# Performance work log

Measured on AMD Instinct MI355X. Metric: run time of the kernel, lower is better.

Reference implementation:

```python
import jax, jax.numpy as jnp
import numpy as np

STATE_DIM = 1024
INPUT_DIM = 1024
OUTPUT_DIM = 1024
BATCH = 8
SEQ = 2048


def setup_inputs() -> dict:
    key = jax.random.key(0)
    k_x, k_a, k_b, k_w, k_bias = jax.random.split(key, 5)
    x = jax.random.normal(k_x, (BATCH, SEQ, INPUT_DIM), dtype=jnp.float32)
    # diagonal transition a in (0, 0.99) for stability
    A = jax.random.uniform(k_a, (STATE_DIM,), dtype=jnp.float32, minval=0.0, maxval=0.99)
    B = jax.random.normal(k_b, (STATE_DIM, INPUT_DIM), dtype=jnp.float32) / np.sqrt(INPUT_DIM)
    W = jax.random.normal(k_w, (OUTPUT_DIM, STATE_DIM), dtype=jnp.float32) / np.sqrt(STATE_DIM)
    b = jax.random.normal(k_bias, (OUTPUT_DIM,), dtype=jnp.float32) * 0.01
    return {"x": x, "A": A, "B": B, "W": W, "b": b}


def reference(x, A, B, W, b):
    # x: [batch, seq, input_dim]
    # Input projection: u_t = B x_t  -> [batch, seq, state_dim]
    u = jnp.einsum('bld,nd->bln', x, B)
    # Diagonal linear recurrence h_t = A * h_{t-1} + u_t via associative scan.
    # Pair representation (a, b) composes as (a1*a2, a2*b1 + b2).
    aa = jnp.broadcast_to(A, u.shape)

    def combine(c1, c2):
        a1, b1 = c1
        a2, b2 = c2
        return a1 * a2, a2 * b1 + b2

    _, h = jax.lax.associative_scan(combine, (aa, u), axis=1)
    # Output projection: [batch, seq, output_dim]
    return jnp.einsum('bln,on->blo', h, W) + b
```

## Files before the change

kernel.cpp:

```cpp
#include <hip/hip_runtime.h>
#include <stdint.h>

#define BATCH 8
#define SEQ 2048
#define DIM 1024
#define MTOT (BATCH * SEQ)
#define NCHUNK 64
#define CLEN (SEQ / NCHUNK)

typedef __attribute__((ext_vector_type(8))) short short8;
typedef __attribute__((ext_vector_type(8))) unsigned short ushort8;
typedef __attribute__((ext_vector_type(4))) float floatx4;


__device__ __forceinline__ unsigned short f2bf(float f) {
  union { float f; unsigned u; } c; c.f = f;
  unsigned u = c.u;
  return (unsigned short)((u + 0x7FFFu + ((u >> 16) & 1u)) >> 16);
}
__device__ __forceinline__ float bf2f(unsigned short h) {
  union { unsigned u; float f; } c; c.u = ((unsigned)h) << 16;
  return c.f;
}

__device__ __forceinline__ void gll16(const void* g, void* l) {
  __builtin_amdgcn_global_load_lds(
      (__attribute__((address_space(1))) void*)(uintptr_t)g,
      (__attribute__((address_space(3))) void*)(uintptr_t)l,
      16, 0, 0);
}


#define XN8 (MTOT * DIM / 8)
#define MN8 (DIM * DIM / 8)

__global__ __launch_bounds__(256) void cast3_kernel(
    const float* __restrict__ x, const float* __restrict__ B,
    const float* __restrict__ W, unsigned short* __restrict__ xb,
    unsigned short* __restrict__ Bb, unsigned short* __restrict__ Wb) {
  int i = blockIdx.x * 256 + threadIdx.x;
  const float* src;
  unsigned short* dst;
  int li;
  if (i < XN8) {
    src = x; dst = xb; li = i;
  } else if (i < XN8 + MN8) {
    src = B; dst = Bb; li = i - XN8;
  } else {
    src = W; dst = Wb; li = i - XN8 - MN8;
  }
  const float4* s4 = (const float4*)src;
  float4 a = s4[2 * li], b = s4[2 * li + 1];
  uint4 o;
  o.x = (unsigned)f2bf(a.x) | ((unsigned)f2bf(a.y) << 16);
  o.y = (unsigned)f2bf(a.z) | ((unsigned)f2bf(a.w) << 16);
  o.z = (unsigned)f2bf(b.x) | ((unsigned)f2bf(b.y) << 16);
  o.w = (unsigned)f2bf(b.z) | ((unsigned)f2bf(b.w) << 16);
  ((uint4*)dst)[li] = o;
}


template <bool OUT_BF16>
__global__ __launch_bounds__(256) void gemm_nt(
    const unsigned short* __restrict__ A,
    const unsigned short* __restrict__ B,
    void* __restrict__ Cp,
    const float* __restrict__ bias,
    int K, int N) {
  __shared__ unsigned short smem[16384];
  unsigned short* sA = smem;
  unsigned short* sB = smem + 8192;

  const int tid = threadIdx.x;
  const int wave = tid >> 6, lane = tid & 63;

  const int id = blockIdx.x;
  const int xcd = id & 7, j = id >> 3;
  const int mt = xcd * 16 + (j >> 3);
  const int nt = j & 7;
  const size_t m0 = (size_t)mt * 128;
  const int n0 = nt * 128;

  floatx4 acc[4][4] = {};

  const int srow = wave * 8 + (lane >> 3);
  const int scol = (((lane & 7) ^ ((lane >> 3) & 7)) * 8);
  const unsigned short* gA = A + (m0 + srow) * (size_t)K + scol;
  const unsigned short* gB = B + ((size_t)n0 + srow) * (size_t)K + scol;
  unsigned short* lA = sA + wave * 8 * 64;
  unsigned short* lB = sB + wave * 8 * 64;

  const int fr = lane & 15;
  const int frs = fr & 7;
  const int kb = lane >> 4;
  const int wm = (wave & 1) * 64, wn = (wave >> 1) * 64;

  for (int kt = 0; kt < K; kt += 64) {
#pragma unroll
    for (int r = 0; r < 4; ++r) {
      gll16(gA + (size_t)r * 32 * K + kt, lA + r * 32 * 64);
      gll16(gB + (size_t)r * 32 * K + kt, lB + r * 32 * 64);
    }
    asm volatile("s_waitcnt vmcnt(0)" ::: "memory");
    __syncthreads();
#pragma unroll
    for (int kk = 0; kk < 64; kk += 32) {
      short8 af[4], bfv[4];
#pragma unroll
      for (int i = 0; i < 4; ++i)
        af[i] = *(const short8*)(sA + (wm + i * 16 + fr) * 64 +
                                 ((((kk >> 3) + kb) ^ frs) * 8));
#pragma unroll
      for (int jj = 0; jj < 4; ++jj)
        bfv[jj] = *(const short8*)(sB + (wn + jj * 16 + fr) * 64 +
                                   ((((kk >> 3) + kb) ^ frs) * 8));
#pragma unroll
      for (int i = 0; i < 4; ++i)
#pragma unroll
        for (int jj = 0; jj < 4; ++jj)
          acc[i][jj] = __builtin_amdgcn_mfma_f32_16x16x32_bf16(
              af[i], bfv[jj], acc[i][jj], 0, 0, 0);
    }
    __syncthreads();
  }

  const int col = lane & 15;
  const int row4 = (lane >> 4) * 4;

  if (OUT_BF16) {
    unsigned short* sC = smem;
#pragma unroll
    for (int i = 0; i < 4; ++i)
#pragma unroll
      for (int jj = 0; jj < 4; ++jj)
#pragma unroll
        for (int r = 0; r < 4; ++r)
          sC[(wm + i * 16 + row4 + r) * 128 + wn + jj * 16 + col] =
              f2bf(acc[i][jj][r]);
    __syncthreads();
    unsigned short* C = (unsigned short*)Cp;
#pragma unroll
    for (int s = 0; s < 8; ++s) {
      int row = wave * 32 + s * 4 + (lane >> 4);
      int c8 = (lane & 15) * 8;
      *(ushort8*)(C + (m0 + row) * (size_t)N + n0 + c8) =
          *(const ushort8*)(sC + row * 128 + c8);
    }
  } else {
    float* C = (float*)Cp;
#pragma unroll
    for (int i = 0; i < 4; ++i) {
#pragma unroll
      for (int jj = 0; jj < 4; ++jj) {
#pragma unroll
        for (int r = 0; r < 4; ++r) {
          size_t m = m0 + wm + i * 16 + row4 + r;
          int n = n0 + wn + jj * 16 + col;
          C[m * N + n] = acc[i][jj][r] + bias[n];
        }
      }
    }
  }
}


__global__ __launch_bounds__(256) void scan_carry(
    const unsigned short* __restrict__ u, const float* __restrict__ A,
    float* __restrict__ carry) {
  const int n0 = threadIdx.x * 8;
  const int c = blockIdx.x * 2 + threadIdx.y;
  const int b = blockIdx.y;
  float a[8], s[8];
  *(float4*)&a[0] = *(const float4*)(A + n0);
  *(float4*)&a[4] = *(const float4*)(A + n0 + 4);
#pragma unroll
  for (int i = 0; i < 8; ++i) s[i] = 0.f;
  size_t base = ((size_t)(b * SEQ + c * CLEN)) * DIM + n0;
#pragma unroll 4
  for (int t = 0; t < CLEN; ++t) {
    ushort8 v = *(const ushort8*)(u + base + (size_t)t * DIM);
#pragma unroll
    for (int i = 0; i < 8; ++i) s[i] = fmaf(a[i], s[i], bf2f(v[i]));
  }
  float* dst = carry + ((size_t)b * NCHUNK + c) * DIM + n0;
  *(float4*)dst = *(float4*)&s[0];
  *(float4*)(dst + 4) = *(float4*)&s[4];
}

__global__ __launch_bounds__(256) void scan_combine(
    float* __restrict__ carry, const float* __restrict__ A) {
  const int id = blockIdx.x * 256 + threadIdx.x;
  const int b = id >> 10, n = id & (DIM - 1);
  float a = A[n];
  float aL = a;
#pragma unroll
  for (int i = 0; i < 5; ++i) aL *= aL;
  float s = 0.f;
  for (int c = 0; c < NCHUNK; ++c) {
    size_t idx = ((size_t)b * NCHUNK + c) * DIM + n;
    float local = carry[idx];
    carry[idx] = s;
    s = fmaf(aL, s, local);
  }
}

__global__ __launch_bounds__(256) void scan_apply(
    unsigned short* __restrict__ u, const float* __restrict__ A,
    const float* __restrict__ carry) {
  const int n0 = threadIdx.x * 8;
  const int c = blockIdx.x * 2 + threadIdx.y;
  const int b = blockIdx.y;
  float a[8], s[8];
  *(float4*)&a[0] = *(const float4*)(A + n0);
  *(float4*)&a[4] = *(const float4*)(A + n0 + 4);
  const float* cin = carry + ((size_t)b * NCHUNK + c) * DIM + n0;
  *(float4*)&s[0] = *(const float4*)cin;
  *(float4*)&s[4] = *(const float4*)(cin + 4);
  size_t base = ((size_t)(b * SEQ + c * CLEN)) * DIM + n0;
#pragma unroll 4
  for (int t = 0; t < CLEN; ++t) {
    size_t idx = base + (size_t)t * DIM;
    ushort8 v = *(const ushort8*)(u + idx);
    ushort8 o;
#pragma unroll
    for (int i = 0; i < 8; ++i) {
      s[i] = fmaf(a[i], s[i], bf2f(v[i]));
      o[i] = f2bf(s[i]);
    }
    *(ushort8*)(u + idx) = o;
  }
}


extern "C" void kernel_launch(void* const* d_in, const int* in_sizes, int n_in,
                              void* d_out, int out_size, void* d_ws,
                              size_t ws_size, hipStream_t stream) {
  const float* x    = (const float*)d_in[0];
  const float* A    = (const float*)d_in[1];
  const float* B    = (const float*)d_in[2];
  const float* W    = (const float*)d_in[3];
  const float* bias = (const float*)d_in[4];

  char* ws = (char*)d_ws;
  unsigned short* xb = (unsigned short*)ws;
  float* carry       = (float*)ws;
  unsigned short* u  = (unsigned short*)(ws + 33554432);
  unsigned short* Bb = (unsigned short*)(ws + 67108864);
  unsigned short* Wb = (unsigned short*)(ws + 69206016);

  cast3_kernel<<<(XN8 + 2 * MN8) / 256, 256, 0, stream>>>(x, B, W, xb, Bb, Wb);

  gemm_nt<true><<<(MTOT / 128) * (DIM / 128), 256, 0, stream>>>(
      xb, Bb, (void*)u, nullptr, DIM, DIM);

  scan_carry<<<dim3(NCHUNK / 2, BATCH), dim3(128, 2), 0, stream>>>(u, A, carry);
  scan_combine<<<(BATCH * DIM) / 256, 256, 0, stream>>>(carry, A);
  scan_apply<<<dim3(NCHUNK / 2, BATCH), dim3(128, 2), 0, stream>>>(u, A, carry);

  gemm_nt<false><<<(MTOT / 128) * (DIM / 128), 256, 0, stream>>>(
      u, Wb, d_out, bias, DIM, DIM);
}
```

Measured before the change: 236.9 us.

## Fuse input GEMM with chunked scan using decoupled lookback and in-kernel x cast

```diff
diff --git a/kernel.cpp b/kernel.cpp
--- a/kernel.cpp
+++ b/kernel.cpp
@@ -5,8 +5,8 @@
 #define SEQ 2048
 #define DIM 1024
 #define MTOT (BATCH * SEQ)
-#define NCHUNK 64
-#define CLEN (SEQ / NCHUNK)
+#define NM 16
+#define NTILE 8
 
 typedef __attribute__((ext_vector_type(8))) short short8;
 typedef __attribute__((ext_vector_type(8))) unsigned short ushort8;
@@ -30,25 +30,25 @@
       16, 0, 0);
 }
 
-
-#define XN8 (MTOT * DIM / 8)
+__device__ __forceinline__ unsigned pkbf(float f1, float f0) {
+  return __builtin_amdgcn_perm(__builtin_bit_cast(unsigned, f1),
+                               __builtin_bit_cast(unsigned, f0), 0x07060302u);
+}
+
+
 #define MN8 (DIM * DIM / 8)
 
-__global__ __launch_bounds__(256) void cast3_kernel(
-    const float* __restrict__ x, const float* __restrict__ B,
-    const float* __restrict__ W, unsigned short* __restrict__ xb,
-    unsigned short* __restrict__ Bb, unsigned short* __restrict__ Wb) {
+__global__ __launch_bounds__(256) void castBW_kernel(
+    const float* __restrict__ B, const float* __restrict__ W,
+    unsigned short* __restrict__ Bb, unsigned short* __restrict__ Wb,
+    unsigned* __restrict__ flags ) {
   int i = blockIdx.x * 256 + threadIdx.x;
-  const float* src;
-  unsigned short* dst;
-  int li;
-  if (i < XN8) {
-    src = x; dst = xb; li = i;
-  } else if (i < XN8 + MN8) {
-    src = B; dst = Bb; li = i - XN8;
-  } else {
-    src = W; dst = Wb; li = i - XN8 - MN8;
-  }
+  if (blockIdx.x == 0) {
+    for (int w = threadIdx.x; w < 1025; w += 256) flags[w] = 0u;
+  }
+  const float* src; unsigned short* dst; int li;
+  if (i < MN8) { src = B; dst = Bb; li = i; }
+  else         { src = W; dst = Wb; li = i - MN8; }
   const float4* s4 = (const float4*)src;
   float4 a = s4[2 * li], b = s4[2 * li + 1];
   uint4 o;
@@ -60,13 +60,194 @@
 }
 
 
-template <bool OUT_BF16>
-__global__ __launch_bounds__(256) void gemm_nt(
+__global__ __launch_bounds__(256) void gemm1_scan(
+    const float* __restrict__ x, const unsigned short* __restrict__ Bb,
+    const float* __restrict__ Adiag, unsigned short* __restrict__ h,
+    float* __restrict__ aggbuf, unsigned* __restrict__ flags,
+    unsigned* __restrict__ ticket) {
+  __shared__ __align__(16) char smem[49152];
+  float* sAf = (float*)smem;
+  unsigned short* sBu = (unsigned short*)(smem + 32768);
+  __shared__ unsigned tkt;
+
+  const int tid = threadIdx.x;
+  const int wave = tid >> 6, lane = tid & 63;
+
+  if (tid == 0) tkt = atomicAdd(ticket, 1u);
+  __syncthreads();
+  const unsigned id = tkt;
+  const int c = id >> 6;
+  const int b = id & 7;
+  const int nt = (id >> 3) & 7;
+  const int mt = b * NM + c;
+  const size_t m0 = (size_t)mt * 128;
+  const int n0 = nt * 128;
+
+  floatx4 acc[4][4] = {};
+
+  unsigned offA[8];
+#pragma unroll
+  for (int r = 0; r < 8; ++r) {
+    int row = wave * 32 + r * 4 + (lane >> 4);
+    int blk = (lane & 15) ^ (row & 15);
+    offA[r] = (unsigned)(row * 4096 + blk * 16);
+  }
+  unsigned offB[4];
+#pragma unroll
+  for (int r = 0; r < 4; ++r) {
+    int row = r * 32 + wave * 8 + (lane >> 3);
+    int blk = (lane & 7) ^ ((lane >> 3) & 7);
+    offB[r] = (unsigned)(row * 2048 + blk * 16);
+  }
+  const char* baseA = (const char*)(x + m0 * 1024);
+  const char* baseB = (const char*)(Bb + (size_t)n0 * 1024);
+
+  const int fr = lane & 15;
+  const int kb = lane >> 4;
+  const int wm = (wave & 1) * 64, wn = (wave >> 1) * 64;
+
+  for (int kt = 0; kt < 1024; kt += 64) {
+#pragma unroll
+    for (int r = 0; r < 8; ++r)
+      gll16(baseA + offA[r], smem + (wave * 32 + r * 4) * 256);
+#pragma unroll
+    for (int r = 0; r < 4; ++r)
+      gll16(baseB + offB[r], (char*)sBu + (wave * 8 + r * 32) * 128);
+    baseA += 256;
+    baseB += 128;
+    asm volatile("s_waitcnt vmcnt(0)" ::: "memory");
+    __syncthreads();
+#pragma unroll
+    for (int kk = 0; kk < 64; kk += 32) {
+      short8 af[4], bfv[4];
+#pragma unroll
+      for (int i = 0; i < 4; ++i) {
+        const float* pA = sAf + (wm + i * 16 + fr) * 64;
+        int bb0 = (kk >> 2) + kb * 2;
+        float4 lo = *(const float4*)(pA + ((bb0 ^ fr) << 2));
+        float4 hi = *(const float4*)(pA + (((bb0 + 1) ^ fr) << 2));
+        union { short8 s; uint4 u; } cv;
+        cv.u.x = pkbf(lo.y, lo.x);
+        cv.u.y = pkbf(lo.w, lo.z);
+        cv.u.z = pkbf(hi.y, hi.x);
+        cv.u.w = pkbf(hi.w, hi.z);
+        af[i] = cv.s;
+      }
+#pragma unroll
+      for (int jj = 0; jj < 4; ++jj)
+        bfv[jj] = *(const short8*)(sBu + (wn + jj * 16 + fr) * 64 +
+                                   ((((kk >> 3) + kb) ^ (fr & 7)) * 8));
+#pragma unroll
+      for (int i = 0; i < 4; ++i)
+#pragma unroll
+        for (int jj = 0; jj < 4; ++jj)
+          acc[i][jj] = __builtin_amdgcn_mfma_f32_16x16x32_bf16(
+              af[i], bfv[jj], acc[i][jj], 0, 0, 0);
+    }
+    __syncthreads();
+  }
+
+  unsigned short* sC = (unsigned short*)smem;
+  float* segsum = (float*)(smem + 32768);
+  float* aLs    = (float*)(smem + 32768 + 1024);
+  float* l2as   = (float*)(smem + 32768 + 1536);
+  float* carryB = (float*)(smem + 32768 + 2048);
+
+  const int col = lane & 15;
+  const int row4 = (lane >> 4) * 4;
+#pragma unroll
+  for (int i = 0; i < 4; ++i)
+#pragma unroll
+    for (int jj = 0; jj < 4; ++jj)
+#pragma unroll
+      for (int r = 0; r < 4; ++r)
+        sC[(wm + i * 16 + row4 + r) * 128 + wn + jj * 16 + col] =
+            f2bf(acc[i][jj][r]);
+  __syncthreads();
+
+  {
+    const int n = tid & 127, seg = tid >> 7;
+    const float a = Adiag[n0 + n];
+    float s = 0.f;
+    int t0 = seg * 64;
+#pragma unroll 8
+    for (int t = 0; t < 64; ++t) {
+      s = fmaf(a, s, bf2f(sC[(t0 + t) * 128 + n]));
+      sC[(t0 + t) * 128 + n] = f2bf(s);
+    }
+    segsum[seg * 128 + n] = s;
+    if (seg == 0) {
+      float a2 = a * a, a4 = a2 * a2, a8 = a4 * a4, a16 = a8 * a8;
+      float a32 = a16 * a16;
+      aLs[n] = a32 * a32;
+      l2as[n] = __builtin_amdgcn_logf(a);
+    }
+  }
+  __syncthreads();
+
+  if (tid < 128) {
+    aggbuf[(size_t)mt * 1024 + n0 + tid] =
+        segsum[128 + tid] + aLs[tid] * segsum[tid];
+  }
+  __syncthreads();
+  if (tid == 0)
+    __hip_atomic_store(&flags[mt * 8 + nt], 1u, __ATOMIC_RELEASE,
+                       __HIP_MEMORY_SCOPE_AGENT);
+
+  if (tid < 128) {
+    float aL128 = aLs[tid] * aLs[tid];
+    float cb = 0.f;
+    for (int p = 0; p < c; ++p) {
+      const int fi = (b * NM + p) * 8 + nt;
+      while (__hip_atomic_load(&flags[fi], __ATOMIC_ACQUIRE,
+                               __HIP_MEMORY_SCOPE_AGENT) == 0u)
+        __builtin_amdgcn_s_sleep(2);
+      cb = fmaf(aL128, cb, aggbuf[(size_t)(b * NM + p) * 1024 + n0 + tid]);
+    }
+    carryB[tid] = cb;
+  }
+  __syncthreads();
+
+  {
+    const int nb = (lane & 15) * 8;
+    const int seg = wave >> 1;
+    float cf[8], l2[8], a4v[8], apow[8];
+#pragma unroll
+    for (int j = 0; j < 8; ++j) {
+      int n = nb + j;
+      float cb = carryB[n];
+      cf[j] = seg ? fmaf(aLs[n], cb, segsum[n]) : cb;
+      l2[j] = l2as[n];
+      float a = Adiag[n0 + n];
+      float a2 = a * a;
+      a4v[j] = a2 * a2;
+    }
+    const int rr0 = (wave & 1) * 32 + (lane >> 4);
+#pragma unroll
+    for (int j = 0; j < 8; ++j)
+      apow[j] = __builtin_amdgcn_exp2f(l2[j] * (float)(rr0 + 1));
+    unsigned short* hout = h + (m0 + wave * 32) * 1024 + n0 + nb;
+#pragma unroll
+    for (int s = 0; s < 8; ++s) {
+      int row = wave * 32 + s * 4 + (lane >> 4);
+      ushort8 loc = *(const ushort8*)(sC + row * 128 + nb);
+      ushort8 o;
+#pragma unroll
+      for (int j = 0; j < 8; ++j) {
+        float v = fmaf(apow[j], cf[j], bf2f(loc[j]));
+        o[j] = f2bf(v);
+        apow[j] *= a4v[j];
+      }
+      *(ushort8*)(hout + (size_t)(s * 4 + (lane >> 4)) * 1024) = o;
+    }
+  }
+}
+
+
+__global__ __launch_bounds__(256) void gemm2(
     const unsigned short* __restrict__ A,
     const unsigned short* __restrict__ B,
-    void* __restrict__ Cp,
-    const float* __restrict__ bias,
-    int K, int N) {
+    float* __restrict__ C, const float* __restrict__ bias) {
   __shared__ unsigned short smem[16384];
   unsigned short* sA = smem;
   unsigned short* sB = smem + 8192;
@@ -85,8 +266,8 @@
 
   const int srow = wave * 8 + (lane >> 3);
   const int scol = (((lane & 7) ^ ((lane >> 3) & 7)) * 8);
-  const unsigned short* gA = A + (m0 + srow) * (size_t)K + scol;
-  const unsigned short* gB = B + ((size_t)n0 + srow) * (size_t)K + scol;
+  const unsigned short* gA = A + (m0 + srow) * 1024 + scol;
+  const unsigned short* gB = B + ((size_t)n0 + srow) * 1024 + scol;
   unsigned short* lA = sA + wave * 8 * 64;
   unsigned short* lB = sB + wave * 8 * 64;
 
@@ -95,11 +276,11 @@
   const int kb = lane >> 4;
   const int wm = (wave & 1) * 64, wn = (wave >> 1) * 64;
 
-  for (int kt = 0; kt < K; kt += 64) {
+  for (int kt = 0; kt < 1024; kt += 64) {
 #pragma unroll
     for (int r = 0; r < 4; ++r) {
-      gll16(gA + (size_t)r * 32 * K + kt, lA + r * 32 * 64);
-      gll16(gB + (size_t)r * 32 * K + kt, lB + r * 32 * 64);
+      gll16(gA + (size_t)r * 32 * 1024 + kt, lA + r * 32 * 64);
+      gll16(gB + (size_t)r * 32 * 1024 + kt, lB + r * 32 * 64);
     }
     asm volatile("s_waitcnt vmcnt(0)" ::: "memory");
     __syncthreads();
@@ -126,109 +307,16 @@
 
   const int col = lane & 15;
   const int row4 = (lane >> 4) * 4;
-
-  if (OUT_BF16) {
-    unsigned short* sC = smem;
-#pragma unroll
-    for (int i = 0; i < 4; ++i)
-#pragma unroll
-      for (int jj = 0; jj < 4; ++jj)
-#pragma unroll
-        for (int r = 0; r < 4; ++r)
-          sC[(wm + i * 16 + row4 + r) * 128 + wn + jj * 16 + col] =
-              f2bf(acc[i][jj][r]);
-    __syncthreads();
-    unsigned short* C = (unsigned short*)Cp;
-#pragma unroll
-    for (int s = 0; s < 8; ++s) {
-      int row = wave * 32 + s * 4 + (lane >> 4);
-      int c8 = (lane & 15) * 8;
-      *(ushort8*)(C + (m0 + row) * (size_t)N + n0 + c8) =
-          *(const ushort8*)(sC + row * 128 + c8);
-    }
-  } else {
-    float* C = (float*)Cp;
-#pragma unroll
-    for (int i = 0; i < 4; ++i) {
-#pragma unroll
-      for (int jj = 0; jj < 4; ++jj) {
-#pragma unroll
-        for (int r = 0; r < 4; ++r) {
-          size_t m = m0 + wm + i * 16 + row4 + r;
-          int n = n0 + wn + jj * 16 + col;
-          C[m * N + n] = acc[i][jj][r] + bias[n];
-        }
+#pragma unroll
+  for (int i = 0; i < 4; ++i)
+#pragma unroll
+    for (int jj = 0; jj < 4; ++jj)
+#pragma unroll
+      for (int r = 0; r < 4; ++r) {
+        size_t m = m0 + wm + i * 16 + row4 + r;
+        int n = n0 + wn + jj * 16 + col;
+        C[m * 1024 + n] = acc[i][jj][r] + bias[n];
       }
-    }
-  }
-}
-
-
-__global__ __launch_bounds__(256) void scan_carry(
-    const unsigned short* __restrict__ u, const float* __restrict__ A,
-    float* __restrict__ carry) {
-  const int n0 = threadIdx.x * 8;
-  const int c = blockIdx.x * 2 + threadIdx.y;
-  const int b = blockIdx.y;
-  float a[8], s[8];
-  *(float4*)&a[0] = *(const float4*)(A + n0);
-  *(float4*)&a[4] = *(const float4*)(A + n0 + 4);
-#pragma unroll
-  for (int i = 0; i < 8; ++i) s[i] = 0.f;
-  size_t base = ((size_t)(b * SEQ + c * CLEN)) * DIM + n0;
-#pragma unroll 4
-  for (int t = 0; t < CLEN; ++t) {
-    ushort8 v = *(const ushort8*)(u + base + (size_t)t * DIM);
-#pragma unroll
-    for (int i = 0; i < 8; ++i) s[i] = fmaf(a[i], s[i], bf2f(v[i]));
-  }
-  float* dst = carry + ((size_t)b * NCHUNK + c) * DIM + n0;
-  *(float4*)dst = *(float4*)&s[0];
-  *(float4*)(dst + 4) = *(float4*)&s[4];
-}
-
-__global__ __launch_bounds__(256) void scan_combine(
-    float* __restrict__ carry, const float* __restrict__ A) {
-  const int id = blockIdx.x * 256 + threadIdx.x;
-  const int b = id >> 10, n = id & (DIM - 1);
-  float a = A[n];
-  float aL = a;
-#pragma unroll
-  for (int i = 0; i < 5; ++i) aL *= aL;
-  float s = 0.f;
-  for (int c = 0; c < NCHUNK; ++c) {
-    size_t idx = ((size_t)b * NCHUNK + c) * DIM + n;
-    float local = carry[idx];
-    carry[idx] = s;
-    s = fmaf(aL, s, local);
-  }
-}
-
-__global__ __launch_bounds__(256) void scan_apply(
-    unsigned short* __restrict__ u, const float* __restrict__ A,
-    const float* __restrict__ carry) {
-  const int n0 = threadIdx.x * 8;
-  const int c = blockIdx.x * 2 + threadIdx.y;
-  const int b = blockIdx.y;
-  float a[8], s[8];
-  *(float4*)&a[0] = *(const float4*)(A + n0);
-  *(float4*)&a[4] = *(const float4*)(A + n0 + 4);
-  const float* cin = carry + ((size_t)b * NCHUNK + c) * DIM + n0;
-  *(float4*)&s[0] = *(const float4*)cin;
-  *(float4*)&s[4] = *(const float4*)(cin + 4);
-  size_t base = ((size_t)(b * SEQ + c * CLEN)) * DIM + n0;
-#pragma unroll 4
-  for (int t = 0; t < CLEN; ++t) {
-    size_t idx = base + (size_t)t * DIM;
-    ushort8 v = *(const ushort8*)(u + idx);
-    ushort8 o;
-#pragma unroll
-    for (int i = 0; i < 8; ++i) {
-      s[i] = fmaf(a[i], s[i], bf2f(v[i]));
-      o[i] = f2bf(s[i]);
-    }
-    *(ushort8*)(u + idx) = o;
-  }
 }
 
 
@@ -242,21 +330,17 @@
   const float* bias = (const float*)d_in[4];
 
   char* ws = (char*)d_ws;
-  unsigned short* xb = (unsigned short*)ws;
-  float* carry       = (float*)ws;
-  unsigned short* u  = (unsigned short*)(ws + 33554432);
-  unsigned short* Bb = (unsigned short*)(ws + 67108864);
-  unsigned short* Wb = (unsigned short*)(ws + 69206016);
-
-  cast3_kernel<<<(XN8 + 2 * MN8) / 256, 256, 0, stream>>>(x, B, W, xb, Bb, Wb);
-
-  gemm_nt<true><<<(MTOT / 128) * (DIM / 128), 256, 0, stream>>>(
-      xb, Bb, (void*)u, nullptr, DIM, DIM);
-
-  scan_carry<<<dim3(NCHUNK / 2, BATCH), dim3(128, 2), 0, stream>>>(u, A, carry);
-  scan_combine<<<(BATCH * DIM) / 256, 256, 0, stream>>>(carry, A);
-  scan_apply<<<dim3(NCHUNK / 2, BATCH), dim3(128, 2), 0, stream>>>(u, A, carry);
-
-  gemm_nt<false><<<(MTOT / 128) * (DIM / 128), 256, 0, stream>>>(
-      u, Wb, d_out, bias, DIM, DIM);
-}
+  unsigned short* hbuf = (unsigned short*)ws;
+  unsigned short* Bb = (unsigned short*)(ws + 33554432);
+  unsigned short* Wb = (unsigned short*)(ws + 35651584);
+  float* aggbuf = (float*)(ws + 37748736);
+  unsigned* flags = (unsigned*)(ws + 38273024);
+  unsigned* ticket = flags + 1024;
+
+  castBW_kernel<<<2 * MN8 / 256, 256, 0, stream>>>(B, W, Bb, Wb, flags);
+
+  gemm1_scan<<<128 * NTILE, 256, 0, stream>>>(x, Bb, A, hbuf, aggbuf, flags,
+                                              ticket);
+
+  gemm2<<<128 * NTILE, 256, 0, stream>>>(hbuf, Wb, (float*)d_out, bias);
+}
```

Measured after the change: 458.6 us. 93.6% more time.

## Replace three-pass chunked scan with single-pass decoupled-lookback scan kernel

Applied to the files above, without the earlier changes.

```diff
diff --git a/kernel.cpp b/kernel.cpp
--- a/kernel.cpp
+++ b/kernel.cpp
@@ -5,8 +5,8 @@
 #define SEQ 2048
 #define DIM 1024
 #define MTOT (BATCH * SEQ)
-#define NCHUNK 64
-#define CLEN (SEQ / NCHUNK)
+#define SC_CH 64
+#define SC_T 32
 
 typedef __attribute__((ext_vector_type(8))) short short8;
 typedef __attribute__((ext_vector_type(8))) unsigned short ushort8;
@@ -37,8 +37,12 @@
 __global__ __launch_bounds__(256) void cast3_kernel(
     const float* __restrict__ x, const float* __restrict__ B,
     const float* __restrict__ W, unsigned short* __restrict__ xb,
-    unsigned short* __restrict__ Bb, unsigned short* __restrict__ Wb) {
+    unsigned short* __restrict__ Bb, unsigned short* __restrict__ Wb,
+    unsigned* __restrict__ flags ) {
   int i = blockIdx.x * 256 + threadIdx.x;
+  if (blockIdx.x == 0) {
+    for (int w = threadIdx.x; w < 544; w += 256) flags[w] = 0u;
+  }
   const float* src;
   unsigned short* dst;
   int li;
@@ -164,70 +168,111 @@
 }
 
 
-__global__ __launch_bounds__(256) void scan_carry(
-    const unsigned short* __restrict__ u, const float* __restrict__ A,
-    float* __restrict__ carry) {
-  const int n0 = threadIdx.x * 8;
-  const int c = blockIdx.x * 2 + threadIdx.y;
-  const int b = blockIdx.y;
-  float a[8], s[8];
-  *(float4*)&a[0] = *(const float4*)(A + n0);
-  *(float4*)&a[4] = *(const float4*)(A + n0 + 4);
-#pragma unroll
-  for (int i = 0; i < 8; ++i) s[i] = 0.f;
-  size_t base = ((size_t)(b * SEQ + c * CLEN)) * DIM + n0;
-#pragma unroll 4
-  for (int t = 0; t < CLEN; ++t) {
+__global__ __launch_bounds__(256, 2) void scan_lb(
+    unsigned short* __restrict__ u, const float* __restrict__ Adiag,
+    float* __restrict__ aggbuf, unsigned* __restrict__ flags,
+    unsigned* __restrict__ ticket) {
+  __shared__ float sHalf0[1024];
+  __shared__ float sCarry[1024];
+  __shared__ unsigned svid;
+
+  const int tid = threadIdx.x;
+  if (tid == 0) svid = atomicAdd(ticket, 1u);
+  __syncthreads();
+  const unsigned vid = svid;
+  const int b = vid & 7;
+  const int c = vid >> 3;
+  const int half = tid >> 7;
+  const int ch0 = (tid & 127) * 8;
+  const int lane = tid & 63;
+
+  float a[8], a16[8], aL[8];
+  *(float4*)&a[0] = *(const float4*)(Adiag + ch0);
+  *(float4*)&a[4] = *(const float4*)(Adiag + ch0 + 4);
+#pragma unroll
+  for (int j = 0; j < 8; ++j) {
+    float t = a[j];
+    t *= t; t *= t; t *= t; t *= t;
+    a16[j] = t;
+    aL[j] = t * t;
+  }
+
+  const size_t base = ((size_t)(b * SEQ + c * SC_T + half * 16)) * DIM + ch0;
+  ushort8 rv[16];
+  float s[8];
+#pragma unroll
+  for (int j = 0; j < 8; ++j) s[j] = 0.f;
+#pragma unroll
+  for (int t = 0; t < 16; ++t) {
     ushort8 v = *(const ushort8*)(u + base + (size_t)t * DIM);
 #pragma unroll
-    for (int i = 0; i < 8; ++i) s[i] = fmaf(a[i], s[i], bf2f(v[i]));
-  }
-  float* dst = carry + ((size_t)b * NCHUNK + c) * DIM + n0;
-  *(float4*)dst = *(float4*)&s[0];
-  *(float4*)(dst + 4) = *(float4*)&s[4];
-}
-
-__global__ __launch_bounds__(256) void scan_combine(
-    float* __restrict__ carry, const float* __restrict__ A) {
-  const int id = blockIdx.x * 256 + threadIdx.x;
-  const int b = id >> 10, n = id & (DIM - 1);
-  float a = A[n];
-  float aL = a;
-#pragma unroll
-  for (int i = 0; i < 5; ++i) aL *= aL;
-  float s = 0.f;
-  for (int c = 0; c < NCHUNK; ++c) {
-    size_t idx = ((size_t)b * NCHUNK + c) * DIM + n;
-    float local = carry[idx];
-    carry[idx] = s;
-    s = fmaf(aL, s, local);
-  }
-}
-
-__global__ __launch_bounds__(256) void scan_apply(
-    unsigned short* __restrict__ u, const float* __restrict__ A,
-    const float* __restrict__ carry) {
-  const int n0 = threadIdx.x * 8;
-  const int c = blockIdx.x * 2 + threadIdx.y;
-  const int b = blockIdx.y;
-  float a[8], s[8];
-  *(float4*)&a[0] = *(const float4*)(A + n0);
-  *(float4*)&a[4] = *(const float4*)(A + n0 + 4);
-  const float* cin = carry + ((size_t)b * NCHUNK + c) * DIM + n0;
-  *(float4*)&s[0] = *(const float4*)cin;
-  *(float4*)&s[4] = *(const float4*)(cin + 4);
-  size_t base = ((size_t)(b * SEQ + c * CLEN)) * DIM + n0;
-#pragma unroll 4
-  for (int t = 0; t < CLEN; ++t) {
-    size_t idx = base + (size_t)t * DIM;
-    ushort8 v = *(const ushort8*)(u + idx);
+    for (int j = 0; j < 8; ++j) {
+      s[j] = fmaf(a[j], s[j], bf2f(v[j]));
+      rv[t][j] = f2bf(s[j]);
+    }
+  }
+
+  if (half == 0) {
+    *(float4*)(sHalf0 + ch0) = *(float4*)&s[0];
+    *(float4*)(sHalf0 + ch0 + 4) = *(float4*)&s[4];
+  }
+  __syncthreads();
+
+  if (half == 1) {
+    float* dst = aggbuf + (size_t)(b * SC_CH + c) * 1024 + ch0;
+#pragma unroll
+    for (int j = 0; j < 8; ++j) dst[j] = fmaf(a16[j], sHalf0[ch0 + j], s[j]);
+  }
+  __threadfence();
+  __syncthreads();
+  if (tid == 0)
+    __hip_atomic_store(&flags[b * SC_CH + c], 1u, __ATOMIC_RELEASE,
+                       __HIP_MEMORY_SCOPE_AGENT);
+
+  if (half == 0) {
+    const bool need = lane < c;
+    const unsigned fi = b * SC_CH + lane;
+    while (true) {
+      unsigned f = need ? __hip_atomic_load(&flags[fi], __ATOMIC_RELAXED,
+                                            __HIP_MEMORY_SCOPE_AGENT)
+                        : 1u;
+      if (__ballot(f == 0u) == 0ull) break;
+      __builtin_amdgcn_s_sleep(1);
+    }
+    __builtin_amdgcn_fence(__ATOMIC_ACQUIRE, "agent");
+
+    float cb[8];
+#pragma unroll
+    for (int j = 0; j < 8; ++j) cb[j] = 0.f;
+    const float* ab = aggbuf + (size_t)(b * SC_CH) * 1024 + ch0;
+    for (int p = 0; p < c; ++p) {
+      float4 g0 = *(const float4*)(ab + (size_t)p * 1024);
+      float4 g1 = *(const float4*)(ab + (size_t)p * 1024 + 4);
+      float g[8] = {g0.x, g0.y, g0.z, g0.w, g1.x, g1.y, g1.z, g1.w};
+#pragma unroll
+      for (int j = 0; j < 8; ++j) cb[j] = fmaf(aL[j], cb[j], g[j]);
+    }
+    *(float4*)(sCarry + ch0) = *(float4*)&cb[0];
+    *(float4*)(sCarry + ch0 + 4) = *(float4*)&cb[4];
+  }
+  __syncthreads();
+
+  float ce[8], apow[8];
+#pragma unroll
+  for (int j = 0; j < 8; ++j) {
+    float C = sCarry[ch0 + j];
+    ce[j] = half ? fmaf(a16[j], C, sHalf0[ch0 + j]) : C;
+    apow[j] = a[j];
+  }
+#pragma unroll
+  for (int t = 0; t < 16; ++t) {
     ushort8 o;
 #pragma unroll
-    for (int i = 0; i < 8; ++i) {
-      s[i] = fmaf(a[i], s[i], bf2f(v[i]));
-      o[i] = f2bf(s[i]);
-    }
-    *(ushort8*)(u + idx) = o;
+    for (int j = 0; j < 8; ++j) {
+      o[j] = f2bf(fmaf(apow[j], ce[j], bf2f(rv[t][j])));
+      apow[j] *= a[j];
+    }
+    *(ushort8*)(u + base + (size_t)t * DIM) = o;
   }
 }
 
@@ -243,20 +288,21 @@
 
   char* ws = (char*)d_ws;
   unsigned short* xb = (unsigned short*)ws;
-  float* carry       = (float*)ws;
-  unsigned short* u  = (unsigned short*)(ws + 33554432);
+  unsigned short* ubuf = (unsigned short*)(ws + 33554432);
   unsigned short* Bb = (unsigned short*)(ws + 67108864);
   unsigned short* Wb = (unsigned short*)(ws + 69206016);
-
-  cast3_kernel<<<(XN8 + 2 * MN8) / 256, 256, 0, stream>>>(x, B, W, xb, Bb, Wb);
+  float* aggbuf = (float*)(ws + 71303168);
+  unsigned* flags = (unsigned*)(ws + 73400320);
+  unsigned* ticket = flags + 512;
+
+  cast3_kernel<<<(XN8 + 2 * MN8) / 256, 256, 0, stream>>>(x, B, W, xb, Bb, Wb,
+                                                          flags);
 
   gemm_nt<true><<<(MTOT / 128) * (DIM / 128), 256, 0, stream>>>(
-      xb, Bb, (void*)u, nullptr, DIM, DIM);
-
-  scan_carry<<<dim3(NCHUNK / 2, BATCH), dim3(128, 2), 0, stream>>>(u, A, carry);
-  scan_combine<<<(BATCH * DIM) / 256, 256, 0, stream>>>(carry, A);
-  scan_apply<<<dim3(NCHUNK / 2, BATCH), dim3(128, 2), 0, stream>>>(u, A, carry);
+      xb, Bb, (void*)ubuf, nullptr, DIM, DIM);
+
+  scan_lb<<<BATCH * SC_CH, 256, 0, stream>>>(ubuf, A, aggbuf, flags, ticket);
 
   gemm_nt<false><<<(MTOT / 128) * (DIM / 128), 256, 0, stream>>>(
-      u, Wb, d_out, bias, DIM, DIM);
-}
+      ubuf, Wb, d_out, bias, DIM, DIM);
+}
```

Measured after the change: 329.1 us. 38.9% more time.

## Fuse local chunk scan into first GEMM epilogue and parallelize carry apply

Applied to the files above, without the earlier changes.

```diff
diff --git a/kernel.cpp b/kernel.cpp
--- a/kernel.cpp
+++ b/kernel.cpp
@@ -5,8 +5,6 @@
 #define SEQ 2048
 #define DIM 1024
 #define MTOT (BATCH * SEQ)
-#define NCHUNK 64
-#define CLEN (SEQ / NCHUNK)
 
 typedef __attribute__((ext_vector_type(8))) short short8;
 typedef __attribute__((ext_vector_type(8))) unsigned short ushort8;
@@ -31,43 +29,40 @@
 }
 
 
-#define XN8 (MTOT * DIM / 8)
-#define MN8 (DIM * DIM / 8)
+#define X4 (MTOT * DIM / 4)
+#define M4 (DIM * DIM / 4)
 
 __global__ __launch_bounds__(256) void cast3_kernel(
     const float* __restrict__ x, const float* __restrict__ B,
     const float* __restrict__ W, unsigned short* __restrict__ xb,
     unsigned short* __restrict__ Bb, unsigned short* __restrict__ Wb) {
   int i = blockIdx.x * 256 + threadIdx.x;
-  const float* src;
-  unsigned short* dst;
+  const float4* s4;
+  uint2* d2;
   int li;
-  if (i < XN8) {
-    src = x; dst = xb; li = i;
-  } else if (i < XN8 + MN8) {
-    src = B; dst = Bb; li = i - XN8;
+  if (i < X4) {
+    s4 = (const float4*)x; d2 = (uint2*)xb; li = i;
+  } else if (i < X4 + M4) {
+    s4 = (const float4*)B; d2 = (uint2*)Bb; li = i - X4;
   } else {
-    src = W; dst = Wb; li = i - XN8 - MN8;
-  }
-  const float4* s4 = (const float4*)src;
-  float4 a = s4[2 * li], b = s4[2 * li + 1];
-  uint4 o;
-  o.x = (unsigned)f2bf(a.x) | ((unsigned)f2bf(a.y) << 16);
-  o.y = (unsigned)f2bf(a.z) | ((unsigned)f2bf(a.w) << 16);
-  o.z = (unsigned)f2bf(b.x) | ((unsigned)f2bf(b.y) << 16);
-  o.w = (unsigned)f2bf(b.z) | ((unsigned)f2bf(b.w) << 16);
-  ((uint4*)dst)[li] = o;
-}
-
-
-template <bool OUT_BF16>
-__global__ __launch_bounds__(256) void gemm_nt(
+    s4 = (const float4*)W; d2 = (uint2*)Wb; li = i - X4 - M4;
+  }
+  float4 v = s4[li];
+  uint2 o;
+  o.x = (unsigned)f2bf(v.x) | ((unsigned)f2bf(v.y) << 16);
+  o.y = (unsigned)f2bf(v.z) | ((unsigned)f2bf(v.w) << 16);
+  d2[li] = o;
+}
+
+
+__global__ __launch_bounds__(256) void gemm1_fused(
     const unsigned short* __restrict__ A,
     const unsigned short* __restrict__ B,
-    void* __restrict__ Cp,
-    const float* __restrict__ bias,
-    int K, int N) {
+    unsigned short* __restrict__ u,
+    const float* __restrict__ Adiag,
+    float* __restrict__ aggbuf) {
   __shared__ unsigned short smem[16384];
+  __shared__ float segsum[2][128];
   unsigned short* sA = smem;
   unsigned short* sB = smem + 8192;
 
@@ -85,8 +80,8 @@
 
   const int srow = wave * 8 + (lane >> 3);
   const int scol = (((lane & 7) ^ ((lane >> 3) & 7)) * 8);
-  const unsigned short* gA = A + (m0 + srow) * (size_t)K + scol;
-  const unsigned short* gB = B + ((size_t)n0 + srow) * (size_t)K + scol;
+  const unsigned short* gA = A + (m0 + srow) * 1024 + scol;
+  const unsigned short* gB = B + ((size_t)n0 + srow) * 1024 + scol;
   unsigned short* lA = sA + wave * 8 * 64;
   unsigned short* lB = sB + wave * 8 * 64;
 
@@ -95,11 +90,11 @@
   const int kb = lane >> 4;
   const int wm = (wave & 1) * 64, wn = (wave >> 1) * 64;
 
-  for (int kt = 0; kt < K; kt += 64) {
+  for (int kt = 0; kt < 1024; kt += 64) {
 #pragma unroll
     for (int r = 0; r < 4; ++r) {
-      gll16(gA + (size_t)r * 32 * K + kt, lA + r * 32 * 64);
-      gll16(gB + (size_t)r * 32 * K + kt, lB + r * 32 * 64);
+      gll16(gA + (size_t)r * 32 * 1024 + kt, lA + r * 32 * 64);
+      gll16(gB + (size_t)r * 32 * 1024 + kt, lB + r * 32 * 64);
     }
     asm volatile("s_waitcnt vmcnt(0)" ::: "memory");
     __syncthreads();
@@ -126,109 +121,191 @@
 
   const int col = lane & 15;
   const int row4 = (lane >> 4) * 4;
-
-  if (OUT_BF16) {
-    unsigned short* sC = smem;
-#pragma unroll
-    for (int i = 0; i < 4; ++i)
-#pragma unroll
-      for (int jj = 0; jj < 4; ++jj)
-#pragma unroll
-        for (int r = 0; r < 4; ++r)
-          sC[(wm + i * 16 + row4 + r) * 128 + wn + jj * 16 + col] =
-              f2bf(acc[i][jj][r]);
-    __syncthreads();
-    unsigned short* C = (unsigned short*)Cp;
-#pragma unroll
-    for (int s = 0; s < 8; ++s) {
-      int row = wave * 32 + s * 4 + (lane >> 4);
-      int c8 = (lane & 15) * 8;
-      *(ushort8*)(C + (m0 + row) * (size_t)N + n0 + c8) =
-          *(const ushort8*)(sC + row * 128 + c8);
-    }
-  } else {
-    float* C = (float*)Cp;
-#pragma unroll
-    for (int i = 0; i < 4; ++i) {
-#pragma unroll
-      for (int jj = 0; jj < 4; ++jj) {
-#pragma unroll
-        for (int r = 0; r < 4; ++r) {
-          size_t m = m0 + wm + i * 16 + row4 + r;
-          int n = n0 + wn + jj * 16 + col;
-          C[m * N + n] = acc[i][jj][r] + bias[n];
-        }
-      }
-    }
-  }
-}
-
-
-__global__ __launch_bounds__(256) void scan_carry(
-    const unsigned short* __restrict__ u, const float* __restrict__ A,
-    float* __restrict__ carry) {
-  const int n0 = threadIdx.x * 8;
-  const int c = blockIdx.x * 2 + threadIdx.y;
-  const int b = blockIdx.y;
-  float a[8], s[8];
-  *(float4*)&a[0] = *(const float4*)(A + n0);
-  *(float4*)&a[4] = *(const float4*)(A + n0 + 4);
-#pragma unroll
-  for (int i = 0; i < 8; ++i) s[i] = 0.f;
-  size_t base = ((size_t)(b * SEQ + c * CLEN)) * DIM + n0;
-#pragma unroll 4
-  for (int t = 0; t < CLEN; ++t) {
-    ushort8 v = *(const ushort8*)(u + base + (size_t)t * DIM);
-#pragma unroll
-    for (int i = 0; i < 8; ++i) s[i] = fmaf(a[i], s[i], bf2f(v[i]));
-  }
-  float* dst = carry + ((size_t)b * NCHUNK + c) * DIM + n0;
-  *(float4*)dst = *(float4*)&s[0];
-  *(float4*)(dst + 4) = *(float4*)&s[4];
-}
-
-__global__ __launch_bounds__(256) void scan_combine(
-    float* __restrict__ carry, const float* __restrict__ A) {
+  unsigned short* sC = smem;
+#pragma unroll
+  for (int i = 0; i < 4; ++i)
+#pragma unroll
+    for (int jj = 0; jj < 4; ++jj)
+#pragma unroll
+      for (int r = 0; r < 4; ++r)
+        sC[(wm + i * 16 + row4 + r) * 128 + wn + jj * 16 + col] =
+            f2bf(acc[i][jj][r]);
+  __syncthreads();
+
+  const int colv = tid & 127;
+  const int seg = tid >> 7;
+  const float a = Adiag[n0 + colv];
+  {
+    float s = 0.f;
+    const int t0 = seg * 64;
+#pragma unroll 8
+    for (int t = 0; t < 64; ++t) {
+      int idx = (t0 + t) * 128 + colv;
+      s = fmaf(a, s, bf2f(sC[idx]));
+      sC[idx] = f2bf(s);
+    }
+    segsum[seg][colv] = s;
+  }
+  __syncthreads();
+
+  {
+    float a2 = a * a, a4 = a2 * a2, a8 = a4 * a4, a16 = a8 * a8;
+    float a32 = a16 * a16, a64 = a32 * a32;
+    const float s0 = segsum[0][colv];
+    const int t0 = 64 + seg * 32;
+    float apow = seg ? a32 * a : a;
+#pragma unroll 8
+    for (int t = 0; t < 32; ++t) {
+      int idx = (t0 + t) * 128 + colv;
+      sC[idx] = f2bf(fmaf(apow, s0, bf2f(sC[idx])));
+      apow *= a;
+    }
+    if (seg)
+      aggbuf[(size_t)mt * 1024 + n0 + colv] =
+          fmaf(a64, s0, segsum[1][colv]);
+  }
+  __syncthreads();
+
+#pragma unroll
+  for (int s = 0; s < 8; ++s) {
+    int row = wave * 32 + s * 4 + (lane >> 4);
+    int c8 = (lane & 15) * 8;
+    *(ushort8*)(u + (m0 + row) * (size_t)1024 + n0 + c8) =
+        *(const ushort8*)(sC + row * 128 + c8);
+  }
+}
+
+
+__global__ __launch_bounds__(256) void combine_kernel(
+    const float* __restrict__ agg, float* __restrict__ carry,
+    const float* __restrict__ Adiag) {
   const int id = blockIdx.x * 256 + threadIdx.x;
   const int b = id >> 10, n = id & (DIM - 1);
-  float a = A[n];
+  float a = Adiag[n];
   float aL = a;
 #pragma unroll
-  for (int i = 0; i < 5; ++i) aL *= aL;
+  for (int i = 0; i < 7; ++i) aL *= aL;
   float s = 0.f;
-  for (int c = 0; c < NCHUNK; ++c) {
-    size_t idx = ((size_t)b * NCHUNK + c) * DIM + n;
-    float local = carry[idx];
+#pragma unroll
+  for (int c = 0; c < 16; ++c) {
+    size_t idx = (size_t)(b * 16 + c) * 1024 + n;
+    float local = agg[idx];
     carry[idx] = s;
     s = fmaf(aL, s, local);
   }
 }
 
-__global__ __launch_bounds__(256) void scan_apply(
-    unsigned short* __restrict__ u, const float* __restrict__ A,
+
+__global__ __launch_bounds__(256) void apply_kernel(
+    unsigned short* __restrict__ u, const float* __restrict__ Adiag,
     const float* __restrict__ carry) {
-  const int n0 = threadIdx.x * 8;
-  const int c = blockIdx.x * 2 + threadIdx.y;
-  const int b = blockIdx.y;
-  float a[8], s[8];
-  *(float4*)&a[0] = *(const float4*)(A + n0);
-  *(float4*)&a[4] = *(const float4*)(A + n0 + 4);
-  const float* cin = carry + ((size_t)b * NCHUNK + c) * DIM + n0;
-  *(float4*)&s[0] = *(const float4*)cin;
-  *(float4*)&s[4] = *(const float4*)(cin + 4);
-  size_t base = ((size_t)(b * SEQ + c * CLEN)) * DIM + n0;
-#pragma unroll 4
-  for (int t = 0; t < CLEN; ++t) {
-    size_t idx = base + (size_t)t * DIM;
-    ushort8 v = *(const ushort8*)(u + idx);
+  const int id = blockIdx.x;
+  const int xcd = id & 7, rem = id >> 3;
+  const int mt = xcd * 16 + (rem >> 4);
+  const int sub = rem & 15;
+  const int tg = threadIdx.x >> 7;
+  const int ch0 = (threadIdx.x & 127) * 8;
+
+  float a[8], cf[8];
+  *(float4*)&a[0] = *(const float4*)(Adiag + ch0);
+  *(float4*)&a[4] = *(const float4*)(Adiag + ch0 + 4);
+  const float* cp = carry + (size_t)mt * 1024 + ch0;
+  *(float4*)&cf[0] = *(const float4*)cp;
+  *(float4*)&cf[4] = *(const float4*)(cp + 4);
+
+  const int tl = sub * 8 + tg * 4;
+  float apow[8];
+#pragma unroll
+  for (int j = 0; j < 8; ++j)
+    apow[j] = __builtin_amdgcn_exp2f(__builtin_amdgcn_logf(a[j]) *
+                                     (float)(tl + 1));
+  const size_t base = ((size_t)mt * 128 + tl) * DIM + ch0;
+#pragma unroll
+  for (int s = 0; s < 4; ++s) {
+    ushort8 v = *(const ushort8*)(u + base + (size_t)s * DIM);
     ushort8 o;
 #pragma unroll
-    for (int i = 0; i < 8; ++i) {
-      s[i] = fmaf(a[i], s[i], bf2f(v[i]));
-      o[i] = f2bf(s[i]);
-    }
-    *(ushort8*)(u + idx) = o;
-  }
+    for (int j = 0; j < 8; ++j) {
+      o[j] = f2bf(fmaf(apow[j], cf[j], bf2f(v[j])));
+      apow[j] *= a[j];
+    }
+    *(ushort8*)(u + base + (size_t)s * DIM) = o;
+  }
+}
+
+
+__global__ __launch_bounds__(256) void gemm2(
+    const unsigned short* __restrict__ A, const unsigned short* __restrict__ B,
+    float* __restrict__ C, const float* __restrict__ bias) {
+  __shared__ unsigned short smem[16384];
+  unsigned short* sA = smem;
+  unsigned short* sB = smem + 8192;
+
+  const int tid = threadIdx.x;
+  const int wave = tid >> 6, lane = tid & 63;
+
+  const int id = blockIdx.x;
+  const int xcd = id & 7, j = id >> 3;
+  const int mt = xcd * 16 + (j >> 3);
+  const int nt = j & 7;
+  const size_t m0 = (size_t)mt * 128;
+  const int n0 = nt * 128;
+
+  floatx4 acc[4][4] = {};
+
+  const int srow = wave * 8 + (lane >> 3);
+  const int scol = (((lane & 7) ^ ((lane >> 3) & 7)) * 8);
+  const unsigned short* gA = A + (m0 + srow) * 1024 + scol;
+  const unsigned short* gB = B + ((size_t)n0 + srow) * 1024 + scol;
+  unsigned short* lA = sA + wave * 8 * 64;
+  unsigned short* lB = sB + wave * 8 * 64;
+
+  const int fr = lane & 15;
+  const int frs = fr & 7;
+  const int kb = lane >> 4;
+  const int wm = (wave & 1) * 64, wn = (wave >> 1) * 64;
+
+  for (int kt = 0; kt < 1024; kt += 64) {
+#pragma unroll
+    for (int r = 0; r < 4; ++r) {
+      gll16(gA + (size_t)r * 32 * 1024 + kt, lA + r * 32 * 64);
+      gll16(gB + (size_t)r * 32 * 1024 + kt, lB + r * 32 * 64);
+    }
+    asm volatile("s_waitcnt vmcnt(0)" ::: "memory");
+    __syncthreads();
+#pragma unroll
+    for (int kk = 0; kk < 64; kk += 32) {
+      short8 af[4], bfv[4];
+#pragma unroll
+      for (int i = 0; i < 4; ++i)
+        af[i] = *(const short8*)(sA + (wm + i * 16 + fr) * 64 +
+                                 ((((kk >> 3) + kb) ^ frs) * 8));
+#pragma unroll
+      for (int jj = 0; jj < 4; ++jj)
+        bfv[jj] = *(const short8*)(sB + (wn + jj * 16 + fr) * 64 +
+                                   ((((kk >> 3) + kb) ^ frs) * 8));
+#pragma unroll
+      for (int i = 0; i < 4; ++i)
+#pragma unroll
+        for (int jj = 0; jj < 4; ++jj)
+          acc[i][jj] = __builtin_amdgcn_mfma_f32_16x16x32_bf16(
+              af[i], bfv[jj], acc[i][jj], 0, 0, 0);
+    }
+    __syncthreads();
+  }
+
+  const int col = lane & 15;
+  const int row4 = (lane >> 4) * 4;
+#pragma unroll
+  for (int i = 0; i < 4; ++i)
+#pragma unroll
+    for (int jj = 0; jj < 4; ++jj)
+#pragma unroll
+      for (int r = 0; r < 4; ++r) {
+        size_t m = m0 + wm + i * 16 + row4 + r;
+        int n = n0 + wn + jj * 16 + col;
+        C[m * 1024 + n] = acc[i][jj][r] + bias[n];
+      }
 }
 
 
@@ -242,21 +319,20 @@
   const float* bias = (const float*)d_in[4];
 
   char* ws = (char*)d_ws;
-  unsigned short* xb = (unsigned short*)ws;
-  float* carry       = (float*)ws;
-  unsigned short* u  = (unsigned short*)(ws + 33554432);
-  unsigned short* Bb = (unsigned short*)(ws + 67108864);
-  unsigned short* Wb = (unsigned short*)(ws + 69206016);
-
-  cast3_kernel<<<(XN8 + 2 * MN8) / 256, 256, 0, stream>>>(x, B, W, xb, Bb, Wb);
-
-  gemm_nt<true><<<(MTOT / 128) * (DIM / 128), 256, 0, stream>>>(
-      xb, Bb, (void*)u, nullptr, DIM, DIM);
-
-  scan_carry<<<dim3(NCHUNK / 2, BATCH), dim3(128, 2), 0, stream>>>(u, A, carry);
-  scan_combine<<<(BATCH * DIM) / 256, 256, 0, stream>>>(carry, A);
-  scan_apply<<<dim3(NCHUNK / 2, BATCH), dim3(128, 2), 0, stream>>>(u, A, carry);
-
-  gemm_nt<false><<<(MTOT / 128) * (DIM / 128), 256, 0, stream>>>(
-      u, Wb, d_out, bias, DIM, DIM);
-}
+  unsigned short* xb   = (unsigned short*)ws;
+  unsigned short* ubuf = (unsigned short*)(ws + 33554432);
+  unsigned short* Bb   = (unsigned short*)(ws + 67108864);
+  unsigned short* Wb   = (unsigned short*)(ws + 69206016);
+  float* aggbuf        = (float*)(ws + 71303168);
+  float* carry         = (float*)(ws + 71827456);
+
+  cast3_kernel<<<(X4 + 2 * M4) / 256, 256, 0, stream>>>(x, B, W, xb, Bb, Wb);
+
+  gemm1_fused<<<1024, 256, 0, stream>>>(xb, Bb, ubuf, A, aggbuf);
+
+  combine_kernel<<<32, 256, 0, stream>>>(aggbuf, carry, A);
+
+  apply_kernel<<<2048, 256, 0, stream>>>(ubuf, A, carry);
+
+  gemm2<<<1024, 256, 0, stream>>>(ubuf, Wb, (float*)d_out, bias);
+}
```

New measurement: 233.5 us. About the same (-1.5%).
